# Optimization experiments

Measured on AMD Instinct MI355X. Metric: run time of the kernel, lower is better.

The kernel has to match this reference:

```python
import jax, jax.numpy as jnp
import numpy as np

TOP_K = 2

def setup_inputs() -> dict:
    key = jax.random.key(0)
    k1, k2 = jax.random.split(key)
    x = jax.random.normal(k1, (2048, 4, 4096), dtype=jnp.float32)
    W = jax.random.normal(k2, (64, 4096), dtype=jnp.float32) * 0.02
    return {"x": x, "W": W}

def reference(x, W):
    # x: (sl, bs, hs) -> tokens: (sl*bs, hs)
    tokens = x.reshape(-1, x.shape[-1])
    # router logits: (sl*bs, num_experts); Linear with no bias => x @ W.T
    logits = jnp.einsum('th,eh->te', tokens, W)
    scores = jax.nn.softmax(logits, axis=-1)
    expert_weights, expert_indices = jax.lax.top_k(scores, TOP_K)
    return expert_weights, expert_indices
```

## Files before the change

### kernel.cpp

```cpp
#include <hip/hip_runtime.h>
#include <hip/hip_bf16.h>
#include <stdint.h>

#define HS 4096
#define NE 64

using half8 = __attribute__((ext_vector_type(8))) _Float16;
using f32x4 = __attribute__((ext_vector_type(4))) float;

constexpr int KSPLIT = 8;
constexpr int KPS    = HS / KSPLIT;
constexpr int WPB    = 8;
constexpr int M_WAVE = 32;
constexpr int M_BLK  = WPB * M_WAVE;

constexpr float XS = 16.f;
constexpr float WSC = 1024.f;
constexpr float INV_SCALE = 1.f / (XS * WSC);

__global__ __launch_bounds__(512, 1)
void router_gemm(const float* __restrict__ x, const float* __restrict__ W,
                 float* __restrict__ ws, int n_tokens)
{
    __shared__ half8 Wl8[(KPS / 8) * 2 * NE];

    const int tid = threadIdx.x;
    const int l   = tid & 63;
    const int wv  = __builtin_amdgcn_readfirstlane(tid >> 6);
    const int g   = l >> 4;
    const int e   = l & 15;
    const int k0  = blockIdx.y * KPS;

    {
        const int se = tid >> 3;
        const int sc = tid & 7;
        #pragma unroll
        for (int j = 0; j < 8; ++j) {
            const float* wp = W + (size_t)se * HS + k0 + sc * 8 + j * 64;
            float4 u = *reinterpret_cast<const float4*>(wp);
            float4 v = *reinterpret_cast<const float4*>(wp + 4);
            const int kg = sc + j * 8;
            float f[8] = {u.x, u.y, u.z, u.w, v.x, v.y, v.z, v.w};
            half8 h, lo;
            #pragma unroll
            for (int i = 0; i < 8; ++i) {
                float s = f[i] * WSC;
                _Float16 hh = (_Float16)s;
                h[i]  = hh;
                lo[i] = (_Float16)(s - (float)hh);
            }
            Wl8[(kg * 2 + 0) * NE + se] = h;
            Wl8[(kg * 2 + 1) * NE + se] = lo;
        }
    }
    __syncthreads();

    const int m0 = blockIdx.x * M_BLK + wv * M_WAVE;
    const float* xr0 = x + (size_t)(m0 + e) * HS + k0 + g * 8;
    const float* xr1 = xr0 + (size_t)16 * HS;

    f32x4 acc[2][4];
    #pragma unroll
    for (int i = 0; i < 2; ++i)
        #pragma unroll
        for (int j = 0; j < 4; ++j) acc[i][j] = (f32x4){0.f, 0.f, 0.f, 0.f};

    float4 c00 = *reinterpret_cast<const float4*>(xr0);
    float4 c01 = *reinterpret_cast<const float4*>(xr0 + 4);
    float4 c10 = *reinterpret_cast<const float4*>(xr1);
    float4 c11 = *reinterpret_cast<const float4*>(xr1 + 4);

    #pragma unroll 2
    for (int ks = 0; ks < KPS / 32; ++ks) {
        float4 n00 = c00, n01 = c01, n10 = c10, n11 = c11;
        if (ks + 1 < KPS / 32) {
            const float* p0 = xr0 + (ks + 1) * 32;
            const float* p1 = xr1 + (ks + 1) * 32;
            n00 = *reinterpret_cast<const float4*>(p0);
            n01 = *reinterpret_cast<const float4*>(p0 + 4);
            n10 = *reinterpret_cast<const float4*>(p1);
            n11 = *reinterpret_cast<const float4*>(p1 + 4);
        }

        const int sb = (ks * 4 + g) * 2;
        half8 bh[4], bl[4];
        #pragma unroll
        for (int nt = 0; nt < 4; ++nt) {
            bh[nt] = Wl8[(sb + 0) * NE + nt * 16 + e];
            bl[nt] = Wl8[(sb + 1) * NE + nt * 16 + e];
        }

        half8 ah0, al0, ah1, al1;
        {
            float f0[8] = {c00.x, c00.y, c00.z, c00.w, c01.x, c01.y, c01.z, c01.w};
            float f1[8] = {c10.x, c10.y, c10.z, c10.w, c11.x, c11.y, c11.z, c11.w};
            #pragma unroll
            for (int i = 0; i < 8; ++i) {
                float s0 = f0[i] * XS; _Float16 h0 = (_Float16)s0;
                ah0[i] = h0; al0[i] = (_Float16)(s0 - (float)h0);
                float s1 = f1[i] * XS; _Float16 h1 = (_Float16)s1;
                ah1[i] = h1; al1[i] = (_Float16)(s1 - (float)h1);
            }
        }

        #pragma unroll
        for (int nt = 0; nt < 4; ++nt) {
            acc[0][nt] = __builtin_amdgcn_mfma_f32_16x16x32_f16(ah0, bh[nt], acc[0][nt], 0, 0, 0);
            acc[0][nt] = __builtin_amdgcn_mfma_f32_16x16x32_f16(al0, bh[nt], acc[0][nt], 0, 0, 0);
            acc[0][nt] = __builtin_amdgcn_mfma_f32_16x16x32_f16(ah0, bl[nt], acc[0][nt], 0, 0, 0);
            acc[1][nt] = __builtin_amdgcn_mfma_f32_16x16x32_f16(ah1, bh[nt], acc[1][nt], 0, 0, 0);
            acc[1][nt] = __builtin_amdgcn_mfma_f32_16x16x32_f16(al1, bh[nt], acc[1][nt], 0, 0, 0);
            acc[1][nt] = __builtin_amdgcn_mfma_f32_16x16x32_f16(ah1, bl[nt], acc[1][nt], 0, 0, 0);
        }

        c00 = n00; c01 = n01; c10 = n10; c11 = n11;
    }

    #pragma unroll
    for (int mt = 0; mt < 2; ++mt)
        #pragma unroll
        for (int nt = 0; nt < 4; ++nt)
            #pragma unroll
            for (int r = 0; r < 4; ++r) {
                const int tok = m0 + mt * 16 + g * 4 + r;
                const int ex  = nt * 16 + e;
                ws[((size_t)blockIdx.y * n_tokens + tok) * NE + ex] = acc[mt][nt][r];
            }
}

__global__ __launch_bounds__(256)
void router_finish(const float* __restrict__ ws, float* __restrict__ out,
                   int n_tokens)
{
    const int lane  = threadIdx.x & 63;
    const int token = blockIdx.x * 4 + (threadIdx.x >> 6);
    if (token >= n_tokens) return;

    float v = 0.f;
    #pragma unroll
    for (int s = 0; s < KSPLIT; ++s)
        v += ws[(size_t)s * n_tokens * NE + (size_t)token * NE + lane];
    v *= INV_SCALE;

    float m1 = v;
    #pragma unroll
    for (int off = 32; off >= 1; off >>= 1) m1 = fmaxf(m1, __shfl_xor(m1, off));
    unsigned long long b1 = __ballot(v == m1);
    int i1 = __ffsll(b1) - 1;

    const float NINF = __int_as_float(0xff800000);
    float vx = (lane == i1) ? NINF : v;
    float m2 = vx;
    #pragma unroll
    for (int off = 32; off >= 1; off >>= 1) m2 = fmaxf(m2, __shfl_xor(m2, off));
    unsigned long long b2 = __ballot(vx == m2);
    int i2 = __ffsll(b2) - 1;

    float s = __expf(v - m1);
    #pragma unroll
    for (int off = 32; off >= 1; off >>= 1) s += __shfl_xor(s, off);

    if (lane == 0) {
        float inv = 1.0f / s;
        out[(size_t)token * 2 + 0] = inv;
        out[(size_t)token * 2 + 1] = __expf(m2 - m1) * inv;
        out[(size_t)n_tokens * 2 + (size_t)token * 2 + 0] = (float)i1;
        out[(size_t)n_tokens * 2 + (size_t)token * 2 + 1] = (float)i2;
    }
}

extern "C" void kernel_launch(void* const* d_in, const int* in_sizes, int n_in,
                              void* d_out, int out_size, void* d_ws, size_t ws_size,
                              hipStream_t stream)
{
    const float* x = (const float*)d_in[0];
    const float* W = (const float*)d_in[1];
    float* out = (float*)d_out;
    float* ws  = (float*)d_ws;

    const int n_tokens = in_sizes[0] / HS;

    dim3 grid1(n_tokens / M_BLK, KSPLIT);
    router_gemm<<<grid1, 512, 0, stream>>>(x, W, ws, n_tokens);

    dim3 grid2((n_tokens + 3) / 4);
    router_finish<<<grid2, 256, 0, stream>>>(ws, out, n_tokens);
}
```

Before: 36.66 us.

## Pre-convert W to split-fp16 once and DMA into LDS; deepen x prefetch

```diff
diff --git a/kernel.cpp b/kernel.cpp
--- a/kernel.cpp
+++ b/kernel.cpp
@@ -13,16 +13,47 @@
 constexpr int WPB    = 8;
 constexpr int M_WAVE = 32;
 constexpr int M_BLK  = WPB * M_WAVE;
-
-constexpr float XS = 16.f;
+constexpr int SLOTS  = (KPS / 8) * 2 * NE;
+
+constexpr float XS  = 16.f;
 constexpr float WSC = 1024.f;
 constexpr float INV_SCALE = 1.f / (XS * WSC);
 
+typedef __attribute__((address_space(3))) uint32_t lds_t;
+typedef const __attribute__((address_space(1))) uint32_t glb_t;
+
+__global__ __launch_bounds__(256)
+void router_wconv(const float* __restrict__ W, half8* __restrict__ w16)
+{
+    const int idx = blockIdx.x * 256 + threadIdx.x;
+    const int e   = idx >> 9;
+    const int kg  = idx & 511;
+    const int s   = kg >> 6;
+    const int kgl = kg & 63;
+    const float* wp = W + (size_t)e * HS + (size_t)kg * 8;
+    float4 u = *reinterpret_cast<const float4*>(wp);
+    float4 v = *reinterpret_cast<const float4*>(wp + 4);
+    float f[8] = {u.x, u.y, u.z, u.w, v.x, v.y, v.z, v.w};
+    half8 h, lo;
+    #pragma unroll
+    for (int i = 0; i < 8; ++i) {
+        float sv = f[i] * WSC;
+        _Float16 hh = (_Float16)sv;
+        h[i]  = hh;
+        lo[i] = (_Float16)(sv - (float)hh);
+    }
+    const size_t base = (size_t)s * SLOTS + (size_t)(kgl * 2) * NE + e;
+    w16[base]      = h;
+    w16[base + NE] = lo;
+}
+
+template<bool PRECONV>
 __global__ __launch_bounds__(512, 1)
 void router_gemm(const float* __restrict__ x, const float* __restrict__ W,
-                 float* __restrict__ ws, int n_tokens)
-{
-    __shared__ half8 Wl8[(KPS / 8) * 2 * NE];
+                 const half8* __restrict__ w16, float* __restrict__ ws,
+                 int n_tokens)
+{
+    __shared__ half8 Wl8[SLOTS];
 
     const int tid = threadIdx.x;
     const int l   = tid & 63;
@@ -31,7 +62,14 @@
     const int e   = l & 15;
     const int k0  = blockIdx.y * KPS;
 
-    {
+    if (PRECONV) {
+        const half8* src = w16 + (size_t)blockIdx.y * SLOTS;
+        #pragma unroll
+        for (int r = 0; r < SLOTS / 512; ++r)
+            __builtin_amdgcn_global_load_lds((glb_t*)(src + r * 512 + tid),
+                                             (lds_t*)&Wl8[r * 512 + tid], 16, 0, 0);
+        asm volatile("s_waitcnt vmcnt(0)" ::: "memory");
+    } else {
         const int se = tid >> 3;
         const int sc = tid & 7;
         #pragma unroll
@@ -65,21 +103,26 @@
         #pragma unroll
         for (int j = 0; j < 4; ++j) acc[i][j] = (f32x4){0.f, 0.f, 0.f, 0.f};
 
-    float4 c00 = *reinterpret_cast<const float4*>(xr0);
-    float4 c01 = *reinterpret_cast<const float4*>(xr0 + 4);
-    float4 c10 = *reinterpret_cast<const float4*>(xr1);
-    float4 c11 = *reinterpret_cast<const float4*>(xr1 + 4);
-
+    float4 a00 = *reinterpret_cast<const float4*>(xr0);
+    float4 a01 = *reinterpret_cast<const float4*>(xr0 + 4);
+    float4 a10 = *reinterpret_cast<const float4*>(xr1);
+    float4 a11 = *reinterpret_cast<const float4*>(xr1 + 4);
+    float4 b00 = *reinterpret_cast<const float4*>(xr0 + 32);
+    float4 b01 = *reinterpret_cast<const float4*>(xr0 + 36);
+    float4 b10 = *reinterpret_cast<const float4*>(xr1 + 32);
+    float4 b11 = *reinterpret_cast<const float4*>(xr1 + 36);
+
+    constexpr int NKS = KPS / 32;
     #pragma unroll 2
-    for (int ks = 0; ks < KPS / 32; ++ks) {
-        float4 n00 = c00, n01 = c01, n10 = c10, n11 = c11;
-        if (ks + 1 < KPS / 32) {
-            const float* p0 = xr0 + (ks + 1) * 32;
-            const float* p1 = xr1 + (ks + 1) * 32;
-            n00 = *reinterpret_cast<const float4*>(p0);
-            n01 = *reinterpret_cast<const float4*>(p0 + 4);
-            n10 = *reinterpret_cast<const float4*>(p1);
-            n11 = *reinterpret_cast<const float4*>(p1 + 4);
+    for (int ks = 0; ks < NKS; ++ks) {
+        float4 d00 = b00, d01 = b01, d10 = b10, d11 = b11;
+        if (ks + 2 < NKS) {
+            const float* p0 = xr0 + (ks + 2) * 32;
+            const float* p1 = xr1 + (ks + 2) * 32;
+            d00 = *reinterpret_cast<const float4*>(p0);
+            d01 = *reinterpret_cast<const float4*>(p0 + 4);
+            d10 = *reinterpret_cast<const float4*>(p1);
+            d11 = *reinterpret_cast<const float4*>(p1 + 4);
         }
 
         const int sb = (ks * 4 + g) * 2;
@@ -92,8 +135,8 @@
 
         half8 ah0, al0, ah1, al1;
         {
-            float f0[8] = {c00.x, c00.y, c00.z, c00.w, c01.x, c01.y, c01.z, c01.w};
-            float f1[8] = {c10.x, c10.y, c10.z, c10.w, c11.x, c11.y, c11.z, c11.w};
+            float f0[8] = {a00.x, a00.y, a00.z, a00.w, a01.x, a01.y, a01.z, a01.w};
+            float f1[8] = {a10.x, a10.y, a10.z, a10.w, a11.x, a11.y, a11.z, a11.w};
             #pragma unroll
             for (int i = 0; i < 8; ++i) {
                 float s0 = f0[i] * XS; _Float16 h0 = (_Float16)s0;
@@ -113,7 +156,8 @@
             acc[1][nt] = __builtin_amdgcn_mfma_f32_16x16x32_f16(ah1, bl[nt], acc[1][nt], 0, 0, 0);
         }
 
-        c00 = n00; c01 = n01; c10 = n10; c11 = n11;
+        a00 = b00; a01 = b01; a10 = b10; a11 = b11;
+        b00 = d00; b01 = d01; b10 = d10; b11 = d11;
     }
 
     #pragma unroll
@@ -176,13 +220,23 @@
     const float* x = (const float*)d_in[0];
     const float* W = (const float*)d_in[1];
     float* out = (float*)d_out;
-    float* ws  = (float*)d_ws;
 
     const int n_tokens = in_sizes[0] / HS;
+    const size_t part_bytes = (size_t)KSPLIT * n_tokens * NE * sizeof(float);
+    const size_t w16_bytes  = (size_t)KSPLIT * SLOTS * sizeof(half8);
+
+    float* ws_part = (float*)d_ws;
+    half8* w16     = (half8*)((char*)d_ws + part_bytes);
+    const bool preconv = ws_size >= part_bytes + w16_bytes;
 
     dim3 grid1(n_tokens / M_BLK, KSPLIT);
-    router_gemm<<<grid1, 512, 0, stream>>>(x, W, ws, n_tokens);
+    if (preconv) {
+        router_wconv<<<NE * (HS / 8) / 256, 256, 0, stream>>>(W, w16);
+        router_gemm<true><<<grid1, 512, 0, stream>>>(x, W, w16, ws_part, n_tokens);
+    } else {
+        router_gemm<false><<<grid1, 512, 0, stream>>>(x, W, w16, ws_part, n_tokens);
+    }
 
     dim3 grid2((n_tokens + 3) / 4);
-    router_finish<<<grid2, 256, 0, stream>>>(ws, out, n_tokens);
-}
+    router_finish<<<grid2, 256, 0, stream>>>(ws_part, out, n_tokens);
+}
```

Measured after the change: 40.05 us. +9.2%, slower.

## Fuse router GEMM and softmax top-k into one kernel with intra-block K split

Applied to the files above, without the earlier changes.

```diff
diff --git a/kernel.cpp b/kernel.cpp
--- a/kernel.cpp
+++ b/kernel.cpp
@@ -8,92 +8,112 @@
 using half8 = __attribute__((ext_vector_type(8))) _Float16;
 using f32x4 = __attribute__((ext_vector_type(4))) float;
 
-constexpr int KSPLIT = 8;
-constexpr int KPS    = HS / KSPLIT;
-constexpr int WPB    = 8;
-constexpr int M_WAVE = 32;
-constexpr int M_BLK  = WPB * M_WAVE;
-
-constexpr float XS = 16.f;
+constexpr int M_BLK = 32;
+constexpr int KCH   = 256;
+constexpr int NCH   = HS / KCH;
+constexpr int NSLOT = (KCH / 8) * 2 * NE;
+
+constexpr float XS  = 16.f;
 constexpr float WSC = 1024.f;
 constexpr float INV_SCALE = 1.f / (XS * WSC);
 
 __global__ __launch_bounds__(512, 1)
-void router_gemm(const float* __restrict__ x, const float* __restrict__ W,
-                 float* __restrict__ ws, int n_tokens)
+void router_fused(const float* __restrict__ x, const float* __restrict__ W,
+                  float* __restrict__ out, int n_tokens)
 {
-    __shared__ half8 Wl8[(KPS / 8) * 2 * NE];
+    __shared__ half8 wbuf[2][NSLOT];
+    float* plds = reinterpret_cast<float*>(&wbuf[0][0]);
 
     const int tid = threadIdx.x;
     const int l   = tid & 63;
     const int wv  = __builtin_amdgcn_readfirstlane(tid >> 6);
     const int g   = l >> 4;
     const int e   = l & 15;
-    const int k0  = blockIdx.y * KPS;
+    const int m0  = blockIdx.x * M_BLK;
+
+    const int we = tid >> 3;
+    const int wc = tid & 7;
+
+    const float* xr0 = x + (size_t)(m0 + e) * HS + wv * 32 + g * 8;
+    const float* xr1 = xr0 + (size_t)16 * HS;
+
+    f32x4 acc[2][4];
+    #pragma unroll
+    for (int i = 0; i < 2; ++i)
+        #pragma unroll
+        for (int j = 0; j < 4; ++j) acc[i][j] = (f32x4){0.f, 0.f, 0.f, 0.f};
+
+    float4 xc00 = *(const float4*)(xr0);
+    float4 xc01 = *(const float4*)(xr0 + 4);
+    float4 xc10 = *(const float4*)(xr1);
+    float4 xc11 = *(const float4*)(xr1 + 4);
+    float4 xn00 = *(const float4*)(xr0 + KCH);
+    float4 xn01 = *(const float4*)(xr0 + KCH + 4);
+    float4 xn10 = *(const float4*)(xr1 + KCH);
+    float4 xn11 = *(const float4*)(xr1 + KCH + 4);
 
     {
-        const int se = tid >> 3;
-        const int sc = tid & 7;
-        #pragma unroll
-        for (int j = 0; j < 8; ++j) {
-            const float* wp = W + (size_t)se * HS + k0 + sc * 8 + j * 64;
-            float4 u = *reinterpret_cast<const float4*>(wp);
-            float4 v = *reinterpret_cast<const float4*>(wp + 4);
-            const int kg = sc + j * 8;
-            float f[8] = {u.x, u.y, u.z, u.w, v.x, v.y, v.z, v.w};
+        const float* wp = W + (size_t)we * HS + wc * 32;
+        float4 wr0 = *(const float4*)(wp +  0), wr1 = *(const float4*)(wp +  4);
+        float4 wr2 = *(const float4*)(wp +  8), wr3 = *(const float4*)(wp + 12);
+        float4 wr4 = *(const float4*)(wp + 16), wr5 = *(const float4*)(wp + 20);
+        float4 wr6 = *(const float4*)(wp + 24), wr7 = *(const float4*)(wp + 28);
+        float4 wq[8] = {wr0, wr1, wr2, wr3, wr4, wr5, wr6, wr7};
+        #pragma unroll
+        for (int kq = 0; kq < 4; ++kq) {
+            float f[8] = {wq[2*kq].x, wq[2*kq].y, wq[2*kq].z, wq[2*kq].w,
+                          wq[2*kq+1].x, wq[2*kq+1].y, wq[2*kq+1].z, wq[2*kq+1].w};
             half8 h, lo;
             #pragma unroll
             for (int i = 0; i < 8; ++i) {
                 float s = f[i] * WSC;
                 _Float16 hh = (_Float16)s;
-                h[i]  = hh;
-                lo[i] = (_Float16)(s - (float)hh);
-            }
-            Wl8[(kg * 2 + 0) * NE + se] = h;
-            Wl8[(kg * 2 + 1) * NE + se] = lo;
+                h[i] = hh; lo[i] = (_Float16)(s - (float)hh);
+            }
+            const int kgl = wc * 4 + kq;
+            wbuf[0][(kgl * 2 + 0) * NE + we] = h;
+            wbuf[0][(kgl * 2 + 1) * NE + we] = lo;
         }
     }
-    __syncthreads();
-
-    const int m0 = blockIdx.x * M_BLK + wv * M_WAVE;
-    const float* xr0 = x + (size_t)(m0 + e) * HS + k0 + g * 8;
-    const float* xr1 = xr0 + (size_t)16 * HS;
-
-    f32x4 acc[2][4];
-    #pragma unroll
-    for (int i = 0; i < 2; ++i)
-        #pragma unroll
-        for (int j = 0; j < 4; ++j) acc[i][j] = (f32x4){0.f, 0.f, 0.f, 0.f};
-
-    float4 c00 = *reinterpret_cast<const float4*>(xr0);
-    float4 c01 = *reinterpret_cast<const float4*>(xr0 + 4);
-    float4 c10 = *reinterpret_cast<const float4*>(xr1);
-    float4 c11 = *reinterpret_cast<const float4*>(xr1 + 4);
-
-    #pragma unroll 2
-    for (int ks = 0; ks < KPS / 32; ++ks) {
-        float4 n00 = c00, n01 = c01, n10 = c10, n11 = c11;
-        if (ks + 1 < KPS / 32) {
-            const float* p0 = xr0 + (ks + 1) * 32;
-            const float* p1 = xr1 + (ks + 1) * 32;
-            n00 = *reinterpret_cast<const float4*>(p0);
-            n01 = *reinterpret_cast<const float4*>(p0 + 4);
-            n10 = *reinterpret_cast<const float4*>(p1);
-            n11 = *reinterpret_cast<const float4*>(p1 + 4);
-        }
-
-        const int sb = (ks * 4 + g) * 2;
-        half8 bh[4], bl[4];
-        #pragma unroll
-        for (int nt = 0; nt < 4; ++nt) {
-            bh[nt] = Wl8[(sb + 0) * NE + nt * 16 + e];
-            bl[nt] = Wl8[(sb + 1) * NE + nt * 16 + e];
-        }
+
+    #pragma unroll 1
+    for (int c = 0; c < NCH; ++c) {
+        const int cur = c & 1;
+        asm volatile("s_waitcnt lgkmcnt(0)\n\ts_barrier" ::: "memory");
+
+        float4 w0, w1, w2, w3, w4, w5, w6, w7;
+        if (c + 1 < NCH) {
+            const float* wp = W + (size_t)we * HS + (c + 1) * KCH + wc * 32;
+            w0 = *(const float4*)(wp +  0); w1 = *(const float4*)(wp +  4);
+            w2 = *(const float4*)(wp +  8); w3 = *(const float4*)(wp + 12);
+            w4 = *(const float4*)(wp + 16); w5 = *(const float4*)(wp + 20);
+            w6 = *(const float4*)(wp + 24); w7 = *(const float4*)(wp + 28);
+        }
+
+        float4 a00 = xc00, a01 = xc01, a10 = xc10, a11 = xc11;
+        xc00 = xn00; xc01 = xn01; xc10 = xn10; xc11 = xn11;
+        if (c + 2 < NCH) {
+            const int off = (c + 2) * KCH;
+            xn00 = *(const float4*)(xr0 + off);
+            xn01 = *(const float4*)(xr0 + off + 4);
+            xn10 = *(const float4*)(xr1 + off);
+            xn11 = *(const float4*)(xr1 + off + 4);
+        }
+
+        const int kb = (wv * 4 + g) * 2;
+        half8 bh0 = wbuf[cur][(kb + 0) * NE +  0 + e];
+        half8 bl0 = wbuf[cur][(kb + 1) * NE +  0 + e];
+        half8 bh1 = wbuf[cur][(kb + 0) * NE + 16 + e];
+        half8 bl1 = wbuf[cur][(kb + 1) * NE + 16 + e];
+        half8 bh2 = wbuf[cur][(kb + 0) * NE + 32 + e];
+        half8 bl2 = wbuf[cur][(kb + 1) * NE + 32 + e];
+        half8 bh3 = wbuf[cur][(kb + 0) * NE + 48 + e];
+        half8 bl3 = wbuf[cur][(kb + 1) * NE + 48 + e];
 
         half8 ah0, al0, ah1, al1;
         {
-            float f0[8] = {c00.x, c00.y, c00.z, c00.w, c01.x, c01.y, c01.z, c01.w};
-            float f1[8] = {c10.x, c10.y, c10.z, c10.w, c11.x, c11.y, c11.z, c11.w};
+            float f0[8] = {a00.x, a00.y, a00.z, a00.w, a01.x, a01.y, a01.z, a01.w};
+            float f1[8] = {a10.x, a10.y, a10.z, a10.w, a11.x, a11.y, a11.z, a11.w};
             #pragma unroll
             for (int i = 0; i < 8; ++i) {
                 float s0 = f0[i] * XS; _Float16 h0 = (_Float16)s0;
@@ -103,69 +123,99 @@
             }
         }
 
-        #pragma unroll
-        for (int nt = 0; nt < 4; ++nt) {
-            acc[0][nt] = __builtin_amdgcn_mfma_f32_16x16x32_f16(ah0, bh[nt], acc[0][nt], 0, 0, 0);
-            acc[0][nt] = __builtin_amdgcn_mfma_f32_16x16x32_f16(al0, bh[nt], acc[0][nt], 0, 0, 0);
-            acc[0][nt] = __builtin_amdgcn_mfma_f32_16x16x32_f16(ah0, bl[nt], acc[0][nt], 0, 0, 0);
-            acc[1][nt] = __builtin_amdgcn_mfma_f32_16x16x32_f16(ah1, bh[nt], acc[1][nt], 0, 0, 0);
-            acc[1][nt] = __builtin_amdgcn_mfma_f32_16x16x32_f16(al1, bh[nt], acc[1][nt], 0, 0, 0);
-            acc[1][nt] = __builtin_amdgcn_mfma_f32_16x16x32_f16(ah1, bl[nt], acc[1][nt], 0, 0, 0);
-        }
-
-        c00 = n00; c01 = n01; c10 = n10; c11 = n11;
+        acc[0][0] = __builtin_amdgcn_mfma_f32_16x16x32_f16(ah0, bh0, acc[0][0], 0, 0, 0);
+        acc[0][0] = __builtin_amdgcn_mfma_f32_16x16x32_f16(al0, bh0, acc[0][0], 0, 0, 0);
+        acc[0][0] = __builtin_amdgcn_mfma_f32_16x16x32_f16(ah0, bl0, acc[0][0], 0, 0, 0);
+        acc[0][1] = __builtin_amdgcn_mfma_f32_16x16x32_f16(ah0, bh1, acc[0][1], 0, 0, 0);
+        acc[0][1] = __builtin_amdgcn_mfma_f32_16x16x32_f16(al0, bh1, acc[0][1], 0, 0, 0);
+        acc[0][1] = __builtin_amdgcn_mfma_f32_16x16x32_f16(ah0, bl1, acc[0][1], 0, 0, 0);
+        acc[0][2] = __builtin_amdgcn_mfma_f32_16x16x32_f16(ah0, bh2, acc[0][2], 0, 0, 0);
+        acc[0][2] = __builtin_amdgcn_mfma_f32_16x16x32_f16(al0, bh2, acc[0][2], 0, 0, 0);
+        acc[0][2] = __builtin_amdgcn_mfma_f32_16x16x32_f16(ah0, bl2, acc[0][2], 0, 0, 0);
+        acc[0][3] = __builtin_amdgcn_mfma_f32_16x16x32_f16(ah0, bh3, acc[0][3], 0, 0, 0);
+        acc[0][3] = __builtin_amdgcn_mfma_f32_16x16x32_f16(al0, bh3, acc[0][3], 0, 0, 0);
+        acc[0][3] = __builtin_amdgcn_mfma_f32_16x16x32_f16(ah0, bl3, acc[0][3], 0, 0, 0);
+        acc[1][0] = __builtin_amdgcn_mfma_f32_16x16x32_f16(ah1, bh0, acc[1][0], 0, 0, 0);
+        acc[1][0] = __builtin_amdgcn_mfma_f32_16x16x32_f16(al1, bh0, acc[1][0], 0, 0, 0);
+        acc[1][0] = __builtin_amdgcn_mfma_f32_16x16x32_f16(ah1, bl0, acc[1][0], 0, 0, 0);
+        acc[1][1] = __builtin_amdgcn_mfma_f32_16x16x32_f16(ah1, bh1, acc[1][1], 0, 0, 0);
+        acc[1][1] = __builtin_amdgcn_mfma_f32_16x16x32_f16(al1, bh1, acc[1][1], 0, 0, 0);
+        acc[1][1] = __builtin_amdgcn_mfma_f32_16x16x32_f16(ah1, bl1, acc[1][1], 0, 0, 0);
+        acc[1][2] = __builtin_amdgcn_mfma_f32_16x16x32_f16(ah1, bh2, acc[1][2], 0, 0, 0);
+        acc[1][2] = __builtin_amdgcn_mfma_f32_16x16x32_f16(al1, bh2, acc[1][2], 0, 0, 0);
+        acc[1][2] = __builtin_amdgcn_mfma_f32_16x16x32_f16(ah1, bl2, acc[1][2], 0, 0, 0);
+        acc[1][3] = __builtin_amdgcn_mfma_f32_16x16x32_f16(ah1, bh3, acc[1][3], 0, 0, 0);
+        acc[1][3] = __builtin_amdgcn_mfma_f32_16x16x32_f16(al1, bh3, acc[1][3], 0, 0, 0);
+        acc[1][3] = __builtin_amdgcn_mfma_f32_16x16x32_f16(ah1, bl3, acc[1][3], 0, 0, 0);
+
+        if (c + 1 < NCH) {
+            float4 wq[8] = {w0, w1, w2, w3, w4, w5, w6, w7};
+            #pragma unroll
+            for (int kq = 0; kq < 4; ++kq) {
+                float f[8] = {wq[2*kq].x, wq[2*kq].y, wq[2*kq].z, wq[2*kq].w,
+                              wq[2*kq+1].x, wq[2*kq+1].y, wq[2*kq+1].z, wq[2*kq+1].w};
+                half8 h, lo;
+                #pragma unroll
+                for (int i = 0; i < 8; ++i) {
+                    float s = f[i] * WSC;
+                    _Float16 hh = (_Float16)s;
+                    h[i] = hh; lo[i] = (_Float16)(s - (float)hh);
+                }
+                const int kgl = wc * 4 + kq;
+                wbuf[cur ^ 1][(kgl * 2 + 0) * NE + we] = h;
+                wbuf[cur ^ 1][(kgl * 2 + 1) * NE + we] = lo;
+            }
+        }
     }
 
+    __syncthreads();
     #pragma unroll
     for (int mt = 0; mt < 2; ++mt)
         #pragma unroll
         for (int nt = 0; nt < 4; ++nt)
             #pragma unroll
             for (int r = 0; r < 4; ++r) {
-                const int tok = m0 + mt * 16 + g * 4 + r;
-                const int ex  = nt * 16 + e;
-                ws[((size_t)blockIdx.y * n_tokens + tok) * NE + ex] = acc[mt][nt][r];
-            }
-}
-
-__global__ __launch_bounds__(256)
-void router_finish(const float* __restrict__ ws, float* __restrict__ out,
-                   int n_tokens)
-{
-    const int lane  = threadIdx.x & 63;
-    const int token = blockIdx.x * 4 + (threadIdx.x >> 6);
-    if (token >= n_tokens) return;
-
-    float v = 0.f;
-    #pragma unroll
-    for (int s = 0; s < KSPLIT; ++s)
-        v += ws[(size_t)s * n_tokens * NE + (size_t)token * NE + lane];
-    v *= INV_SCALE;
-
-    float m1 = v;
-    #pragma unroll
-    for (int off = 32; off >= 1; off >>= 1) m1 = fmaxf(m1, __shfl_xor(m1, off));
-    unsigned long long b1 = __ballot(v == m1);
-    int i1 = __ffsll(b1) - 1;
-
-    const float NINF = __int_as_float(0xff800000);
-    float vx = (lane == i1) ? NINF : v;
-    float m2 = vx;
-    #pragma unroll
-    for (int off = 32; off >= 1; off >>= 1) m2 = fmaxf(m2, __shfl_xor(m2, off));
-    unsigned long long b2 = __ballot(vx == m2);
-    int i2 = __ffsll(b2) - 1;
-
-    float s = __expf(v - m1);
-    #pragma unroll
-    for (int off = 32; off >= 1; off >>= 1) s += __shfl_xor(s, off);
-
-    if (lane == 0) {
-        float inv = 1.0f / s;
-        out[(size_t)token * 2 + 0] = inv;
-        out[(size_t)token * 2 + 1] = __expf(m2 - m1) * inv;
-        out[(size_t)n_tokens * 2 + (size_t)token * 2 + 0] = (float)i1;
-        out[(size_t)n_tokens * 2 + (size_t)token * 2 + 1] = (float)i2;
+                const int tloc = mt * 16 + g * 4 + r;
+                const int ef   = nt * 16 + e;
+                plds[wv * 2176 + tloc * 68 + ef] = acc[mt][nt][r];
+            }
+    __syncthreads();
+
+    #pragma unroll 1
+    for (int jj = 0; jj < 4; ++jj) {
+        const int tloc = wv * 4 + jj;
+        float v = 0.f;
+        #pragma unroll
+        for (int s = 0; s < 8; ++s)
+            v += plds[s * 2176 + tloc * 68 + l];
+        v *= INV_SCALE;
+
+        float m1 = v;
+        #pragma unroll
+        for (int off = 32; off >= 1; off >>= 1) m1 = fmaxf(m1, __shfl_xor(m1, off));
+        unsigned long long b1 = __ballot(v == m1);
+        int i1 = __ffsll(b1) - 1;
+
+        const float NINF = __int_as_float(0xff800000);
+        float vx = (l == i1) ? NINF : v;
+        float m2 = vx;
+        #pragma unroll
+        for (int off = 32; off >= 1; off >>= 1) m2 = fmaxf(m2, __shfl_xor(m2, off));
+        unsigned long long b2 = __ballot(vx == m2);
+        int i2 = __ffsll(b2) - 1;
+
+        float s = __expf(v - m1);
+        #pragma unroll
+        for (int off = 32; off >= 1; off >>= 1) s += __shfl_xor(s, off);
+
+        if (l == 0) {
+            const int tok = m0 + tloc;
+            float inv = 1.0f / s;
+            out[(size_t)tok * 2 + 0] = inv;
+            out[(size_t)tok * 2 + 1] = __expf(m2 - m1) * inv;
+            out[(size_t)n_tokens * 2 + (size_t)tok * 2 + 0] = (float)i1;
+            out[(size_t)n_tokens * 2 + (size_t)tok * 2 + 1] = (float)i2;
+        }
     }
 }
 
@@ -176,13 +226,8 @@
     const float* x = (const float*)d_in[0];
     const float* W = (const float*)d_in[1];
     float* out = (float*)d_out;
-    float* ws  = (float*)d_ws;
 
     const int n_tokens = in_sizes[0] / HS;
-
-    dim3 grid1(n_tokens / M_BLK, KSPLIT);
-    router_gemm<<<grid1, 512, 0, stream>>>(x, W, ws, n_tokens);
-
-    dim3 grid2((n_tokens + 3) / 4);
-    router_finish<<<grid2, 256, 0, stream>>>(ws, out, n_tokens);
+    dim3 grid(n_tokens / M_BLK);
+    router_fused<<<grid, 512, 0, stream>>>(x, W, out, n_tokens);
 }
```

Result: slower. 66.78 us, median of 4 (+82.1%).

## Fuse router GEMM and top-k finish via cooperative grid sync, swizzle LDS

Applied to the files above, without the earlier changes.

```diff
diff --git a/kernel.cpp b/kernel.cpp
--- a/kernel.cpp
+++ b/kernel.cpp
@@ -1,7 +1,10 @@
 #include <hip/hip_runtime.h>
+#include <hip/hip_cooperative_groups.h>
 #include <hip/hip_bf16.h>
 #include <stdint.h>
 
+namespace cg = cooperative_groups;
+
 #define HS 4096
 #define NE 64
 
@@ -10,19 +13,17 @@
 
 constexpr int KSPLIT = 8;
 constexpr int KPS    = HS / KSPLIT;
-constexpr int WPB    = 8;
-constexpr int M_WAVE = 32;
-constexpr int M_BLK  = WPB * M_WAVE;
-
-constexpr float XS = 16.f;
+constexpr int M_BLK  = 256;
+
+constexpr float XS  = 16.f;
 constexpr float WSC = 1024.f;
 constexpr float INV_SCALE = 1.f / (XS * WSC);
 
 __global__ __launch_bounds__(512, 1)
-void router_gemm(const float* __restrict__ x, const float* __restrict__ W,
-                 float* __restrict__ ws, int n_tokens)
+void router_all(const float* __restrict__ x, const float* __restrict__ W,
+                float* __restrict__ ws, float* __restrict__ out, int n_tokens)
 {
-    __shared__ half8 Wl8[(KPS / 8) * 2 * NE];
+    __shared__ half8 Wl8[128 * NE];
 
     const int tid = threadIdx.x;
     const int l   = tid & 63;
@@ -31,31 +32,34 @@
     const int e   = l & 15;
     const int k0  = blockIdx.y * KPS;
 
-    {
-        const int se = tid >> 3;
-        const int sc = tid & 7;
-        #pragma unroll
-        for (int j = 0; j < 8; ++j) {
-            const float* wp = W + (size_t)se * HS + k0 + sc * 8 + j * 64;
-            float4 u = *reinterpret_cast<const float4*>(wp);
-            float4 v = *reinterpret_cast<const float4*>(wp + 4);
-            const int kg = sc + j * 8;
-            float f[8] = {u.x, u.y, u.z, u.w, v.x, v.y, v.z, v.w};
-            half8 h, lo;
-            #pragma unroll
-            for (int i = 0; i < 8; ++i) {
-                float s = f[i] * WSC;
-                _Float16 hh = (_Float16)s;
-                h[i]  = hh;
-                lo[i] = (_Float16)(s - (float)hh);
-            }
-            Wl8[(kg * 2 + 0) * NE + se] = h;
-            Wl8[(kg * 2 + 1) * NE + se] = lo;
-        }
-    }
-    __syncthreads();
-
-    const int m0 = blockIdx.x * M_BLK + wv * M_WAVE;
+    const int se = tid >> 3;
+    const int sc = tid & 7;
+    const float* wrow = W + (size_t)se * HS + k0 + sc * 8;
+
+    float4 u0 = *(const float4*)(wrow +   0), v0 = *(const float4*)(wrow +   4);
+    float4 u1 = *(const float4*)(wrow +  64), v1 = *(const float4*)(wrow +  68);
+    float4 u2 = *(const float4*)(wrow + 128), v2 = *(const float4*)(wrow + 132);
+    float4 u3 = *(const float4*)(wrow + 192), v3 = *(const float4*)(wrow + 196);
+    float4 u4 = *(const float4*)(wrow + 256), v4 = *(const float4*)(wrow + 260);
+    float4 u5 = *(const float4*)(wrow + 320), v5 = *(const float4*)(wrow + 324);
+    float4 u6 = *(const float4*)(wrow + 384), v6 = *(const float4*)(wrow + 388);
+    float4 u7 = *(const float4*)(wrow + 448), v7 = *(const float4*)(wrow + 452);
+
+    auto cvt_store = [&](float4 u, float4 v, int kgl) {
+        float f[8] = {u.x, u.y, u.z, u.w, v.x, v.y, v.z, v.w};
+        half8 h, lo;
+        #pragma unroll
+        for (int i = 0; i < 8; ++i) {
+            float s = f[i] * WSC;
+            _Float16 hh = (_Float16)s;
+            h[i] = hh; lo[i] = (_Float16)(s - (float)hh);
+        }
+        const int base = (kgl * 2) * NE + (se ^ (kgl & 7));
+        Wl8[base]      = h;
+        Wl8[base + NE] = lo;
+    };
+
+    const int m0 = blockIdx.x * M_BLK + wv * 32;
     const float* xr0 = x + (size_t)(m0 + e) * HS + k0 + g * 8;
     const float* xr1 = xr0 + (size_t)16 * HS;
 
@@ -65,55 +69,85 @@
         #pragma unroll
         for (int j = 0; j < 4; ++j) acc[i][j] = (f32x4){0.f, 0.f, 0.f, 0.f};
 
-    float4 c00 = *reinterpret_cast<const float4*>(xr0);
-    float4 c01 = *reinterpret_cast<const float4*>(xr0 + 4);
-    float4 c10 = *reinterpret_cast<const float4*>(xr1);
-    float4 c11 = *reinterpret_cast<const float4*>(xr1 + 4);
-
-    #pragma unroll 2
-    for (int ks = 0; ks < KPS / 32; ++ks) {
-        float4 n00 = c00, n01 = c01, n10 = c10, n11 = c11;
-        if (ks + 1 < KPS / 32) {
-            const float* p0 = xr0 + (ks + 1) * 32;
-            const float* p1 = xr1 + (ks + 1) * 32;
-            n00 = *reinterpret_cast<const float4*>(p0);
-            n01 = *reinterpret_cast<const float4*>(p0 + 4);
-            n10 = *reinterpret_cast<const float4*>(p1);
-            n11 = *reinterpret_cast<const float4*>(p1 + 4);
-        }
-
-        const int sb = (ks * 4 + g) * 2;
-        half8 bh[4], bl[4];
-        #pragma unroll
-        for (int nt = 0; nt < 4; ++nt) {
-            bh[nt] = Wl8[(sb + 0) * NE + nt * 16 + e];
-            bl[nt] = Wl8[(sb + 1) * NE + nt * 16 + e];
-        }
-
-        half8 ah0, al0, ah1, al1;
-        {
-            float f0[8] = {c00.x, c00.y, c00.z, c00.w, c01.x, c01.y, c01.z, c01.w};
-            float f1[8] = {c10.x, c10.y, c10.z, c10.w, c11.x, c11.y, c11.z, c11.w};
-            #pragma unroll
-            for (int i = 0; i < 8; ++i) {
-                float s0 = f0[i] * XS; _Float16 h0 = (_Float16)s0;
-                ah0[i] = h0; al0[i] = (_Float16)(s0 - (float)h0);
-                float s1 = f1[i] * XS; _Float16 h1 = (_Float16)s1;
-                ah1[i] = h1; al1[i] = (_Float16)(s1 - (float)h1);
+    float4 a00 = *(const float4*)(xr0),      a01 = *(const float4*)(xr0 + 4);
+    float4 a10 = *(const float4*)(xr1),      a11 = *(const float4*)(xr1 + 4);
+    float4 b00 = *(const float4*)(xr0 + 32), b01 = *(const float4*)(xr0 + 36);
+    float4 b10 = *(const float4*)(xr1 + 32), b11 = *(const float4*)(xr1 + 36);
+
+    #pragma unroll 1
+    for (int half = 0; half < 2; ++half) {
+        if (half == 0) {
+            cvt_store(u0, v0, sc);       cvt_store(u1, v1, sc + 8);
+            cvt_store(u2, v2, sc + 16);  cvt_store(u3, v3, sc + 24);
+        } else {
+            cvt_store(u4, v4, sc + 32);  cvt_store(u5, v5, sc + 40);
+            cvt_store(u6, v6, sc + 48);  cvt_store(u7, v7, sc + 56);
+        }
+        __syncthreads();
+
+        #pragma unroll 2
+        for (int ks = half * 8; ks < half * 8 + 8; ++ks) {
+            float4 d00 = b00, d01 = b01, d10 = b10, d11 = b11;
+            if (ks + 2 < 16) {
+                const float* p0 = xr0 + (ks + 2) * 32;
+                const float* p1 = xr1 + (ks + 2) * 32;
+                d00 = *(const float4*)(p0); d01 = *(const float4*)(p0 + 4);
+                d10 = *(const float4*)(p1); d11 = *(const float4*)(p1 + 4);
             }
-        }
-
-        #pragma unroll
-        for (int nt = 0; nt < 4; ++nt) {
-            acc[0][nt] = __builtin_amdgcn_mfma_f32_16x16x32_f16(ah0, bh[nt], acc[0][nt], 0, 0, 0);
-            acc[0][nt] = __builtin_amdgcn_mfma_f32_16x16x32_f16(al0, bh[nt], acc[0][nt], 0, 0, 0);
-            acc[0][nt] = __builtin_amdgcn_mfma_f32_16x16x32_f16(ah0, bl[nt], acc[0][nt], 0, 0, 0);
-            acc[1][nt] = __builtin_amdgcn_mfma_f32_16x16x32_f16(ah1, bh[nt], acc[1][nt], 0, 0, 0);
-            acc[1][nt] = __builtin_amdgcn_mfma_f32_16x16x32_f16(al1, bh[nt], acc[1][nt], 0, 0, 0);
-            acc[1][nt] = __builtin_amdgcn_mfma_f32_16x16x32_f16(ah1, bl[nt], acc[1][nt], 0, 0, 0);
-        }
-
-        c00 = n00; c01 = n01; c10 = n10; c11 = n11;
+
+            const int kgl = ks * 4 + g;
+            const int rb  = kgl * 2;
+            const int sw  = kgl & 7;
+            half8 bh0 = Wl8[(rb + 0) * NE + (( 0 + e) ^ sw)];
+            half8 bl0 = Wl8[(rb + 1) * NE + (( 0 + e) ^ sw)];
+            half8 bh1 = Wl8[(rb + 0) * NE + ((16 + e) ^ sw)];
+            half8 bl1 = Wl8[(rb + 1) * NE + ((16 + e) ^ sw)];
+            half8 bh2 = Wl8[(rb + 0) * NE + ((32 + e) ^ sw)];
+            half8 bl2 = Wl8[(rb + 1) * NE + ((32 + e) ^ sw)];
+            half8 bh3 = Wl8[(rb + 0) * NE + ((48 + e) ^ sw)];
+            half8 bl3 = Wl8[(rb + 1) * NE + ((48 + e) ^ sw)];
+
+            half8 ah0, al0, ah1, al1;
+            {
+                float f0[8] = {a00.x, a00.y, a00.z, a00.w, a01.x, a01.y, a01.z, a01.w};
+                float f1[8] = {a10.x, a10.y, a10.z, a10.w, a11.x, a11.y, a11.z, a11.w};
+                #pragma unroll
+                for (int i = 0; i < 8; ++i) {
+                    float s0 = f0[i] * XS; _Float16 h0 = (_Float16)s0;
+                    ah0[i] = h0; al0[i] = (_Float16)(s0 - (float)h0);
+                    float s1 = f1[i] * XS; _Float16 h1 = (_Float16)s1;
+                    ah1[i] = h1; al1[i] = (_Float16)(s1 - (float)h1);
+                }
+            }
+
+            acc[0][0] = __builtin_amdgcn_mfma_f32_16x16x32_f16(ah0, bh0, acc[0][0], 0, 0, 0);
+            acc[0][0] = __builtin_amdgcn_mfma_f32_16x16x32_f16(al0, bh0, acc[0][0], 0, 0, 0);
+            acc[0][0] = __builtin_amdgcn_mfma_f32_16x16x32_f16(ah0, bl0, acc[0][0], 0, 0, 0);
+            acc[0][1] = __builtin_amdgcn_mfma_f32_16x16x32_f16(ah0, bh1, acc[0][1], 0, 0, 0);
+            acc[0][1] = __builtin_amdgcn_mfma_f32_16x16x32_f16(al0, bh1, acc[0][1], 0, 0, 0);
+            acc[0][1] = __builtin_amdgcn_mfma_f32_16x16x32_f16(ah0, bl1, acc[0][1], 0, 0, 0);
+            acc[0][2] = __builtin_amdgcn_mfma_f32_16x16x32_f16(ah0, bh2, acc[0][2], 0, 0, 0);
+            acc[0][2] = __builtin_amdgcn_mfma_f32_16x16x32_f16(al0, bh2, acc[0][2], 0, 0, 0);
+            acc[0][2] = __builtin_amdgcn_mfma_f32_16x16x32_f16(ah0, bl2, acc[0][2], 0, 0, 0);
+            acc[0][3] = __builtin_amdgcn_mfma_f32_16x16x32_f16(ah0, bh3, acc[0][3], 0, 0, 0);
+            acc[0][3] = __builtin_amdgcn_mfma_f32_16x16x32_f16(al0, bh3, acc[0][3], 0, 0, 0);
+            acc[0][3] = __builtin_amdgcn_mfma_f32_16x16x32_f16(ah0, bl3, acc[0][3], 0, 0, 0);
+            acc[1][0] = __builtin_amdgcn_mfma_f32_16x16x32_f16(ah1, bh0, acc[1][0], 0, 0, 0);
+            acc[1][0] = __builtin_amdgcn_mfma_f32_16x16x32_f16(al1, bh0, acc[1][0], 0, 0, 0);
+            acc[1][0] = __builtin_amdgcn_mfma_f32_16x16x32_f16(ah1, bl0, acc[1][0], 0, 0, 0);
+            acc[1][1] = __builtin_amdgcn_mfma_f32_16x16x32_f16(ah1, bh1, acc[1][1], 0, 0, 0);
+            acc[1][1] = __builtin_amdgcn_mfma_f32_16x16x32_f16(al1, bh1, acc[1][1], 0, 0, 0);
+            acc[1][1] = __builtin_amdgcn_mfma_f32_16x16x32_f16(ah1, bl1, acc[1][1], 0, 0, 0);
+            acc[1][2] = __builtin_amdgcn_mfma_f32_16x16x32_f16(ah1, bh2, acc[1][2], 0, 0, 0);
+            acc[1][2] = __builtin_amdgcn_mfma_f32_16x16x32_f16(al1, bh2, acc[1][2], 0, 0, 0);
+            acc[1][2] = __builtin_amdgcn_mfma_f32_16x16x32_f16(ah1, bl2, acc[1][2], 0, 0, 0);
+            acc[1][3] = __builtin_amdgcn_mfma_f32_16x16x32_f16(ah1, bh3, acc[1][3], 0, 0, 0);
+            acc[1][3] = __builtin_amdgcn_mfma_f32_16x16x32_f16(al1, bh3, acc[1][3], 0, 0, 0);
+            acc[1][3] = __builtin_amdgcn_mfma_f32_16x16x32_f16(ah1, bl3, acc[1][3], 0, 0, 0);
+
+            a00 = b00; a01 = b01; a10 = b10; a11 = b11;
+            b00 = d00; b01 = d01; b10 = d10; b11 = d11;
+        }
     }
 
     #pragma unroll
@@ -126,46 +160,47 @@
                 const int ex  = nt * 16 + e;
                 ws[((size_t)blockIdx.y * n_tokens + tok) * NE + ex] = acc[mt][nt][r];
             }
-}
-
-__global__ __launch_bounds__(256)
-void router_finish(const float* __restrict__ ws, float* __restrict__ out,
-                   int n_tokens)
-{
-    const int lane  = threadIdx.x & 63;
-    const int token = blockIdx.x * 4 + (threadIdx.x >> 6);
-    if (token >= n_tokens) return;
-
-    float v = 0.f;
-    #pragma unroll
-    for (int s = 0; s < KSPLIT; ++s)
-        v += ws[(size_t)s * n_tokens * NE + (size_t)token * NE + lane];
-    v *= INV_SCALE;
-
-    float m1 = v;
-    #pragma unroll
-    for (int off = 32; off >= 1; off >>= 1) m1 = fmaxf(m1, __shfl_xor(m1, off));
-    unsigned long long b1 = __ballot(v == m1);
-    int i1 = __ffsll(b1) - 1;
-
-    const float NINF = __int_as_float(0xff800000);
-    float vx = (lane == i1) ? NINF : v;
-    float m2 = vx;
-    #pragma unroll
-    for (int off = 32; off >= 1; off >>= 1) m2 = fmaxf(m2, __shfl_xor(m2, off));
-    unsigned long long b2 = __ballot(vx == m2);
-    int i2 = __ffsll(b2) - 1;
-
-    float s = __expf(v - m1);
-    #pragma unroll
-    for (int off = 32; off >= 1; off >>= 1) s += __shfl_xor(s, off);
-
-    if (lane == 0) {
-        float inv = 1.0f / s;
-        out[(size_t)token * 2 + 0] = inv;
-        out[(size_t)token * 2 + 1] = __expf(m2 - m1) * inv;
-        out[(size_t)n_tokens * 2 + (size_t)token * 2 + 0] = (float)i1;
-        out[(size_t)n_tokens * 2 + (size_t)token * 2 + 1] = (float)i2;
+
+    __threadfence();
+    cg::this_grid().sync();
+
+    const int tb = blockIdx.y * gridDim.x + blockIdx.x;
+    #pragma unroll 1
+    for (int jj = 0; jj < 4; ++jj) {
+        const int token = tb * 32 + wv * 4 + jj;
+        if (token >= n_tokens) break;
+
+        float v = 0.f;
+        #pragma unroll
+        for (int s = 0; s < KSPLIT; ++s)
+            v += ws[((size_t)s * n_tokens + token) * NE + l];
+        v *= INV_SCALE;
+
+        float m1 = v;
+        #pragma unroll
+        for (int off = 32; off >= 1; off >>= 1) m1 = fmaxf(m1, __shfl_xor(m1, off));
+        unsigned long long b1 = __ballot(v == m1);
+        int i1 = __ffsll(b1) - 1;
+
+        const float NINF = __int_as_float(0xff800000);
+        float vx = (l == i1) ? NINF : v;
+        float m2 = vx;
+        #pragma unroll
+        for (int off = 32; off >= 1; off >>= 1) m2 = fmaxf(m2, __shfl_xor(m2, off));
+        unsigned long long b2 = __ballot(vx == m2);
+        int i2 = __ffsll(b2) - 1;
+
+        float s = __expf(v - m1);
+        #pragma unroll
+        for (int off = 32; off >= 1; off >>= 1) s += __shfl_xor(s, off);
+
+        if (l == 0) {
+            float inv = 1.0f / s;
+            out[(size_t)token * 2 + 0] = inv;
+            out[(size_t)token * 2 + 1] = __expf(m2 - m1) * inv;
+            out[(size_t)n_tokens * 2 + (size_t)token * 2 + 0] = (float)i1;
+            out[(size_t)n_tokens * 2 + (size_t)token * 2 + 1] = (float)i2;
+        }
     }
 }
 
@@ -178,11 +213,9 @@
     float* out = (float*)d_out;
     float* ws  = (float*)d_ws;
 
-    const int n_tokens = in_sizes[0] / HS;
-
-    dim3 grid1(n_tokens / M_BLK, KSPLIT);
-    router_gemm<<<grid1, 512, 0, stream>>>(x, W, ws, n_tokens);
-
-    dim3 grid2((n_tokens + 3) / 4);
-    router_finish<<<grid2, 256, 0, stream>>>(ws, out, n_tokens);
+    int n_tokens = in_sizes[0] / HS;
+    dim3 grid(n_tokens / M_BLK, KSPLIT);
+
+    void* args[] = {(void*)&x, (void*)&W, (void*)&ws, (void*)&out, (void*)&n_tokens};
+    hipLaunchCooperativeKernel((void*)router_all, grid, dim3(512), args, 0, stream);
 }
```

After: 134.0 us. +265.4%, slower.
